# Kernel tuning notes

Hardware: AMD Instinct MI355X
Metric: run time of the kernel (lower is better)

The kernel has to match this reference:

```python
import jax, jax.numpy as jnp
import numpy as np

NUM_PM = 254
NUM_VM = 768
SEQ = NUM_PM + NUM_VM + 2  # 1024
H = 8
D = 256
DH = D // H
FF = 1024
L = 3
B = 8
PM_COV = 16
VM_COV = 16


def _ln(x, g, b, eps=1e-5):
    m = jnp.mean(x, axis=-1, keepdims=True)
    v = jnp.mean((x - m) ** 2, axis=-1, keepdims=True)
    return (x - m) * jax.lax.rsqrt(v + eps) * g + b


def setup_inputs() -> dict:
    key = jax.random.key(0)
    ks = jax.random.split(key, 32)
    n = lambda k, s: (jax.random.normal(k, s, dtype=jnp.float32) * 0.02)
    return {
        "vm_states": jax.random.normal(ks[0], (B, NUM_VM, VM_COV), dtype=jnp.float32),
        "num_step_states": jax.random.uniform(ks[1], (B, 1, 1), dtype=jnp.float32),
        "pm_states": jax.random.normal(ks[2], (B, NUM_PM, PM_COV), dtype=jnp.float32),
        "vm_pm_relation": jax.random.randint(ks[3], (B, SEQ - 2, 1), 0, NUM_PM),
        "num_vms_mask": jnp.zeros((B, NUM_VM), dtype=bool),
        "pm_W": n(ks[4], (PM_COV, D)), "pm_b": jnp.zeros((D,), jnp.float32),
        "vm_W": n(ks[5], (VM_COV, D)), "vm_b": jnp.zeros((D,), jnp.float32),
        "Wqkv": n(ks[6], (L, D, 3 * D)), "bqkv": jnp.zeros((L, 3 * D), jnp.float32),
        "Wo": n(ks[7], (L, D, D)), "bo": jnp.zeros((L, D), jnp.float32),
        "ln1_g": jnp.ones((L, D), jnp.float32), "ln1_b": jnp.zeros((L, D), jnp.float32),
        "ln2_g": jnp.ones((L, D), jnp.float32), "ln2_b": jnp.zeros((L, D), jnp.float32),
        "W1": n(ks[8], (L, D, FF)), "b1": jnp.zeros((L, FF), jnp.float32),
        "W2": n(ks[9], (L, FF, D)), "b2": jnp.zeros((L, D), jnp.float32),
        "out_W": n(ks[10], (D, 1)), "out_b": jnp.zeros((1,), jnp.float32),
        "crit_W": n(ks[11], (D, 1)), "crit_b": jnp.zeros((1,), jnp.float32),
    }


def reference(vm_states, num_step_states, pm_states, vm_pm_relation, num_vms_mask,
              pm_W, pm_b, vm_W, vm_b, Wqkv, bqkv, Wo, bo,
              ln1_g, ln1_b, ln2_g, ln2_b, W1, b1, W2, b2,
              out_W, out_b, crit_W, crit_b):
    b = vm_states.shape[0]
    # --- relation-based sparse mask: True = blocked ---
    r = vm_pm_relation[:, :, 0]                              # [b, SEQ-2]
    inner = r[:, :, None] != r[:, None, :]                   # [b, SEQ-2, SEQ-2]
    local = jnp.ones((b, SEQ, SEQ), dtype=bool)
    local = local.at[:, 0, 0].set(False)
    local = local.at[:, -1, -1].set(False)
    local = local.at[:, 1:-1, 1:-1].set(inner)
    pad = jnp.zeros((b, SEQ), dtype=bool).at[:, 1 + NUM_PM:-1].set(num_vms_mask)
    bias = jnp.where(local | pad[:, None, :], -1e9, 0.0)[:, None]  # [b,1,SEQ,SEQ]
    # --- encode ---
    src = jnp.concatenate([jnp.tile(num_step_states, (1, 1, D)),
                           pm_states @ pm_W + pm_b], axis=1)       # [b, NUM_PM+1, D]
    critic_tok = -jnp.ones((b, 1, D), dtype=vm_states.dtype)
    tgt = jnp.concatenate([vm_states @ vm_W + vm_b, critic_tok], axis=1)  # [b, NUM_VM+1, D]
    x = jnp.concatenate([src, tgt], axis=1)                   # [b, SEQ, D]
    scale = 1.0 / np.sqrt(DH)
    for i in range(L):
        # pre-norm masked self-attention
        h = _ln(x, ln1_g[i], ln1_b[i])
        qkv = h @ Wqkv[i] + bqkv[i]
        q, k, v = [t.reshape(b, SEQ, H, DH) for t in jnp.split(qkv, 3, axis=-1)]
        scores = jnp.einsum('bqhd,bkhd->bhqk', q, k) * scale + bias
        attn = jax.nn.softmax(scores, axis=-1)
        o = jnp.einsum('bhqk,bkhd->bqhd', attn, v).reshape(b, SEQ, D)
        x = x + o @ Wo[i] + bo[i]
        # pre-norm gelu FFN
        h2 = _ln(x, ln2_g[i], ln2_b[i])
        x = x + jax.nn.gelu(h2 @ W1[i] + b1[i]) @ W2[i] + b2[i]
    tgt_out = x[:, NUM_PM + 1:]                               # [b, NUM_VM+1, D]
    score = (tgt_out[:, :-1] @ out_W + out_b)[..., 0]         # [b, NUM_VM]
    critic_score = tgt_out[:, -1] @ crit_W + crit_b           # [b, 1]
    return jnp.concatenate([score, critic_score], axis=1)     # [b, NUM_VM+1]
```

## Files before the change

kernel.cpp:

```cpp
#include <hip/hip_runtime.h>
#include <hip/hip_bf16.h>
#include <math.h>

#define NUM_PM 254
#define NUM_VM 768
#define SEQQ   1024
#define NH     8
#define DD     256
#define DH     32
#define FF     1024
#define NB     8
#define MROWS  (NB*SEQQ)

typedef unsigned short u16;
typedef __attribute__((ext_vector_type(8))) short bf16x8;
typedef __attribute__((ext_vector_type(4))) float f32x4;

__device__ __forceinline__ float bf2f(u16 u){
    union { float f; unsigned int i; } c; c.i = ((unsigned int)u) << 16; return c.f;
}
__device__ __forceinline__ u16 f2bf(float f){
    union { float f; unsigned int u; } c; c.f = f;
    unsigned int r = c.u + 0x7FFFu + ((c.u >> 16) & 1u);
    return (u16)(r >> 16);
}
__device__ __forceinline__ float gelu_tanh(float x){
    float x3 = x*x*x;
    float t = tanhf(0.7978845608028654f*(x + 0.044715f*x3));
    return 0.5f*x*(1.0f+t);
}

#define GLOAD16(gp, lp) __builtin_amdgcn_global_load_lds( \
    (const __attribute__((address_space(1))) void*)(gp), \
    (__attribute__((address_space(3))) void*)(lp), 16, 0, 0)

__global__ void embed_kernel(const float* __restrict__ vm_states,
                             const float* __restrict__ num_step,
                             const float* __restrict__ pm_states,
                             const float* __restrict__ pm_W, const float* __restrict__ pm_b,
                             const float* __restrict__ vm_W, const float* __restrict__ vm_b,
                             float* __restrict__ x)
{
    int row = blockIdx.x*4 + (threadIdx.x>>6);
    int lane = threadIdx.x & 63;
    int b = row >> 10, s = row & 1023;
    int col = lane*4;
    float4 out;
    if (s == 0){
        float v = num_step[b]; out = (float4){v,v,v,v};
    } else if (s == SEQQ-1){
        out = (float4){-1.f,-1.f,-1.f,-1.f};
    } else {
        const float* in; const float* W; const float* bias;
        if (s <= NUM_PM){ in = pm_states + (size_t)(b*NUM_PM + s-1)*16; W = pm_W; bias = pm_b; }
        else            { in = vm_states + (size_t)(b*NUM_VM + (s-1-NUM_PM))*16; W = vm_W; bias = vm_b; }
        float4 i0 = *(const float4*)in,      i1 = *(const float4*)(in+4);
        float4 i2 = *(const float4*)(in+8),  i3 = *(const float4*)(in+12);
        float in16[16] = {i0.x,i0.y,i0.z,i0.w, i1.x,i1.y,i1.z,i1.w,
                          i2.x,i2.y,i2.z,i2.w, i3.x,i3.y,i3.z,i3.w};
        out = *(const float4*)&bias[col];
        #pragma unroll
        for (int k=0;k<16;k++){
            float4 w4 = *(const float4*)&W[k*DD + col];
            out.x = fmaf(in16[k], w4.x, out.x);
            out.y = fmaf(in16[k], w4.y, out.y);
            out.z = fmaf(in16[k], w4.z, out.z);
            out.w = fmaf(in16[k], w4.w, out.w);
        }
    }
    *(float4*)&x[(size_t)row*DD + col] = out;
}

__global__ void tcast_all_kernel(const float* __restrict__ Wqkv, const float* __restrict__ Wo,
                                 const float* __restrict__ W1,   const float* __restrict__ W2,
                                 u16* __restrict__ wq, u16* __restrict__ wo,
                                 u16* __restrict__ w1, u16* __restrict__ w2)
{
    __shared__ float t[32][33];
    int id = blockIdx.x;
    const float* in; u16* out; int K, N, layer, tile;
    if (id < 576)       { in=Wqkv; out=wq; K=256;  N=768;  layer=id/192; tile=id%192; }
    else if (id < 768)  { id-=576;  in=Wo; out=wo; K=256;  N=256;  layer=id/64;  tile=id%64;  }
    else if (id < 1536) { id-=768;  in=W1; out=w1; K=256;  N=1024; layer=id/256; tile=id%256; }
    else                { id-=1536; in=W2; out=w2; K=1024; N=256;  layer=id/256; tile=id%256; }
    int ntx = N/32;
    int n0 = (tile % ntx)*32, k0 = (tile / ntx)*32;
    size_t lofs = (size_t)layer * K * N;
    int tx = threadIdx.x & 31, ty = threadIdx.x >> 5;
    #pragma unroll
    for (int i=0;i<4;i++)
        t[ty + i*8][tx] = in[lofs + (size_t)(k0 + ty + i*8)*N + n0 + tx];
    __syncthreads();
    #pragma unroll
    for (int i=0;i<4;i++)
        out[lofs + (size_t)(n0 + ty + i*8)*K + k0 + tx] = f2bf(t[tx][ty + i*8]);
}

__global__ void ln_kernel(const float* __restrict__ x, const float* __restrict__ g,
                          const float* __restrict__ bta, u16* __restrict__ out)
{
    int row = blockIdx.x*4 + (threadIdx.x>>6);
    int lane = threadIdx.x & 63;
    const float4 v = *(const float4*)&x[(size_t)row*DD + lane*4];
    float s1 = v.x+v.y+v.z+v.w;
    float s2 = fmaf(v.x,v.x, fmaf(v.y,v.y, fmaf(v.z,v.z, v.w*v.w)));
    #pragma unroll
    for (int off=1; off<64; off<<=1){ s1 += __shfl_xor(s1,off); s2 += __shfl_xor(s2,off); }
    float m    = s1*(1.0f/DD);
    float var  = s2*(1.0f/DD) - m*m;
    float rstd = rsqrtf(var + 1e-5f);
    float4 g4 = *(const float4*)&g[lane*4];
    float4 b4 = *(const float4*)&bta[lane*4];
    short4 o;
    o.x = (short)f2bf((v.x-m)*rstd*g4.x + b4.x);
    o.y = (short)f2bf((v.y-m)*rstd*g4.y + b4.y);
    o.z = (short)f2bf((v.z-m)*rstd*g4.z + b4.z);
    o.w = (short)f2bf((v.w-m)*rstd*g4.w + b4.w);
    *(short4*)&out[(size_t)row*DD + lane*4] = o;
}

template<int EPI>
__launch_bounds__(256)
__global__ void mgemm_kernel(const u16* __restrict__ A, const u16* __restrict__ Bt,
                             const float* __restrict__ bias, u16* __restrict__ C,
                             int N, int K)
{
    __shared__ u16 As[2][128][32];
    __shared__ u16 Bs[2][128][32];
    int tid = threadIdx.x;
    int wid = tid >> 6, lane = tid & 63;
    int wr = wid >> 1, wc = wid & 1;
    int row0 = blockIdx.y*128, col0 = blockIdx.x*128;
    int l15 = lane & 15, lh = lane >> 4;

    int srow = wid*32 + (lane>>2);
    int skof = (lane&3)*8;
    const u16* Ag = A  + (size_t)(row0 + srow)*K + skof;
    const u16* Bg = Bt + (size_t)(col0 + srow)*K + skof;

#define STAGE_M(buf, k0) do{ \
    GLOAD16(Ag + (k0),          &As[buf][wid*32][0]);    \
    GLOAD16(Ag + (k0) + 16*K,   &As[buf][wid*32+16][0]); \
    GLOAD16(Bg + (k0),          &Bs[buf][wid*32][0]);    \
    GLOAD16(Bg + (k0) + 16*K,   &Bs[buf][wid*32+16][0]); }while(0)

    f32x4 acc[4][4] = {};
    int nk = K >> 5;
    STAGE_M(0, 0);
    __syncthreads();
    for (int kt = 0; kt < nk; kt++){
        int cur = kt & 1;
        if (kt+1 < nk) STAGE_M(cur^1, (kt+1)*32);
        bf16x8 af[4], bfv[4];
        #pragma unroll
        for (int f=0; f<4; f++){
            af[f]  = *(const bf16x8*)&As[cur][wr*64 + f*16 + l15][lh*8];
            bfv[f] = *(const bf16x8*)&Bs[cur][wc*64 + f*16 + l15][lh*8];
        }
        #pragma unroll
        for (int i=0;i<4;i++)
            #pragma unroll
            for (int j=0;j<4;j++)
                acc[i][j] = __builtin_amdgcn_mfma_f32_16x16x32_bf16(af[i], bfv[j], acc[i][j], 0,0,0);
        __syncthreads();
    }
#undef STAGE_M

    #pragma unroll
    for (int i=0;i<4;i++){
        #pragma unroll
        for (int j=0;j<4;j++){
            int col = col0 + wc*64 + j*16 + l15;
            float bb = bias[col];
            #pragma unroll
            for (int r=0;r<4;r++){
                int row = row0 + wr*64 + i*16 + lh*4 + r;
                float v = acc[i][j][r] + bb;
                if (EPI==2) v = gelu_tanh(v);
                C[(size_t)row*N + col] = f2bf(v);
            }
        }
    }
}

__launch_bounds__(256)
__global__ void mgemm2_kernel(const u16* __restrict__ A, const u16* __restrict__ Bt,
                              const float* __restrict__ bias, const float* __restrict__ res,
                              float* __restrict__ C, int N, int K)
{
    __shared__ u16 As[2][64][32];
    __shared__ u16 Bs[2][128][32];
    int tid = threadIdx.x;
    int wid = tid >> 6, lane = tid & 63;
    int wr = wid >> 1, wc = wid & 1;
    int row0 = blockIdx.y*64, col0 = blockIdx.x*128;
    int l15 = lane & 15, lh = lane >> 4;

    int srowA = wid*16 + (lane>>2);
    int srowB = wid*32 + (lane>>2);
    int skof  = (lane&3)*8;
    const u16* Ag = A  + (size_t)(row0 + srowA)*K + skof;
    const u16* Bg = Bt + (size_t)(col0 + srowB)*K + skof;

#define STAGE_M2(buf, k0) do{ \
    GLOAD16(Ag + (k0),          &As[buf][wid*16][0]);    \
    GLOAD16(Bg + (k0),          &Bs[buf][wid*32][0]);    \
    GLOAD16(Bg + (k0) + 16*K,   &Bs[buf][wid*32+16][0]); }while(0)

    f32x4 acc[2][4] = {};
    int nk = K >> 5;
    STAGE_M2(0, 0);
    __syncthreads();
    for (int kt = 0; kt < nk; kt++){
        int cur = kt & 1;
        if (kt+1 < nk) STAGE_M2(cur^1, (kt+1)*32);
        bf16x8 af[2], bfv[4];
        #pragma unroll
        for (int i=0;i<2;i++)
            af[i] = *(const bf16x8*)&As[cur][wr*32 + i*16 + l15][lh*8];
        #pragma unroll
        for (int j=0;j<4;j++)
            bfv[j] = *(const bf16x8*)&Bs[cur][wc*64 + j*16 + l15][lh*8];
        #pragma unroll
        for (int i=0;i<2;i++)
            #pragma unroll
            for (int j=0;j<4;j++)
                acc[i][j] = __builtin_amdgcn_mfma_f32_16x16x32_bf16(af[i], bfv[j], acc[i][j], 0,0,0);
        __syncthreads();
    }
#undef STAGE_M2

    #pragma unroll
    for (int i=0;i<2;i++){
        #pragma unroll
        for (int j=0;j<4;j++){
            int col = col0 + wc*64 + j*16 + l15;
            float bb = bias[col];
            #pragma unroll
            for (int r=0;r<4;r++){
                int row = row0 + wr*32 + i*16 + lh*4 + r;
                size_t idx = (size_t)row*N + col;
                C[idx] = acc[i][j][r] + bb + res[idx];
            }
        }
    }
}

__global__ void group_build_kernel(const int* __restrict__ rel, const unsigned char* __restrict__ mask,
                                   int* __restrict__ counts, int* __restrict__ offs,
                                   int* __restrict__ members)
{
    __shared__ int cntS[256], offS[256], wsum[4];
    int b = blockIdx.x, tid = threadIdx.x;
    if (tid < 256) cntS[tid] = 0;
    __syncthreads();
    int s = tid, c = -1, p = -1;
    bool valid = (s != 0) && (s != SEQQ-1);
    if (valid && s >= 1+NUM_PM && mask[b*NUM_VM + (s-1-NUM_PM)]) valid = false;
    if (valid){
        c = rel[b*(SEQQ-2) + s-1];
        p = atomicAdd(&cntS[c], 1);
    }
    __syncthreads();
    if (tid < 256){
        int v = cntS[tid];
        int incl = v;
        #pragma unroll
        for (int d=1; d<64; d<<=1){
            int n = __shfl_up(incl, d);
            if ((tid & 63) >= d) incl += n;
        }
        offS[tid] = incl - v;
        if ((tid & 63) == 63) wsum[tid>>6] = incl;
    }
    __syncthreads();
    if (tid < 256){
        int w = tid >> 6, base = 0;
        #pragma unroll
        for (int i=0;i<4;i++) if (i < w) base += wsum[i];
        offS[tid] += base;
    }
    __syncthreads();
    if (valid) members[b*SEQQ + offS[c] + p] = s;
    if (tid < 256){
        counts[b*256 + tid] = cntS[tid];
        offs[b*256 + tid]   = offS[tid];
    }
}

__launch_bounds__(256)
__global__ void attn_kernel(const u16* __restrict__ qkv, const int* __restrict__ rel,
                            const int* __restrict__ counts, const int* __restrict__ offs,
                            const int* __restrict__ members, u16* __restrict__ o)
{
    int gq = blockIdx.x*4 + (threadIdx.x >> 6);
    int lane = threadIdx.x & 63;
    int b = gq >> 10, s = gq & 1023;
    const float scale = 0.17677669529663687f;

    const u16* base = qkv + (size_t)(b*SEQQ + s)*768 + lane*4;
    short4 q4i = *(const short4*)base;
    float qx = bf2f((u16)q4i.x)*scale, qy = bf2f((u16)q4i.y)*scale,
          qz = bf2f((u16)q4i.z)*scale, qw = bf2f((u16)q4i.w)*scale;

    int cnt; const int* mlist = nullptr;
    if (s == 0 || s == SEQQ-1) { cnt = 1; }
    else {
        int c = rel[b*(SEQQ-2) + s-1];
        cnt   = counts[b*256 + c];
        mlist = members + b*SEQQ + offs[b*256 + c];
    }

    float m_run = -1e30f, l_run = 0.f;
    float ax=0.f, ay=0.f, az=0.f, aw=0.f;
    for (int j0 = 0; j0 < cnt; j0 += 4){
        short4 k4[4], v4[4];
        #pragma unroll
        for (int k=0;k<4;k++){
            int jj = j0 + k; jj = (jj < cnt) ? jj : (cnt-1);
            int mi = mlist ? mlist[jj] : s;
            const u16* kb = qkv + (size_t)(b*SEQQ + mi)*768 + 256 + lane*4;
            k4[k] = *(const short4*)kb;
            v4[k] = *(const short4*)(kb + 256);
        }
        #pragma unroll
        for (int k=0;k<4;k++){
            if (j0 + k < cnt){
                float sc = qx*bf2f((u16)k4[k].x) + qy*bf2f((u16)k4[k].y)
                         + qz*bf2f((u16)k4[k].z) + qw*bf2f((u16)k4[k].w);
                sc += __shfl_xor(sc, 1);
                sc += __shfl_xor(sc, 2);
                sc += __shfl_xor(sc, 4);
                float mn = fmaxf(m_run, sc);
                float corr = __expf(m_run - mn);
                float p = __expf(sc - mn);
                l_run = l_run*corr + p;
                ax = ax*corr + p*bf2f((u16)v4[k].x);
                ay = ay*corr + p*bf2f((u16)v4[k].y);
                az = az*corr + p*bf2f((u16)v4[k].z);
                aw = aw*corr + p*bf2f((u16)v4[k].w);
                m_run = mn;
            }
        }
    }
    float inv = (l_run > 0.f) ? 1.0f/l_run : 0.f;
    u16* orow = o + (size_t)(b*SEQQ + s)*DD + lane*4;
    short4 outv;
    outv.x = (short)f2bf(ax*inv); outv.y = (short)f2bf(ay*inv);
    outv.z = (short)f2bf(az*inv); outv.w = (short)f2bf(aw*inv);
    *(short4*)orow = outv;
}

__global__ void out_kernel(const float* __restrict__ x,
                           const float* __restrict__ out_W, const float* __restrict__ out_b,
                           const float* __restrict__ crit_W, const float* __restrict__ crit_b,
                           float* __restrict__ out)
{
    int gidx = blockIdx.x*4 + (threadIdx.x>>6);
    int lane = threadIdx.x & 63;
    if (gidx >= NB*769) return;
    int b = gidx / 769, j = gidx % 769;
    int srow; const float* Wp; float bb;
    if (j < 768){ srow = b*SEQQ + 1 + NUM_PM + j; Wp = out_W; bb = out_b[0]; }
    else        { srow = b*SEQQ + SEQQ-1;         Wp = crit_W; bb = crit_b[0]; }
    const float* xr = x + (size_t)srow*DD;
    float4 xv = *(const float4*)&xr[lane*4];
    float4 wv = *(const float4*)&Wp[lane*4];
    float sdot = xv.x*wv.x + xv.y*wv.y + xv.z*wv.z + xv.w*wv.w;
    #pragma unroll
    for (int off=32; off; off>>=1) sdot += __shfl_down(sdot, off);
    if (lane==0) out[gidx] = sdot + bb;
}

extern "C" void kernel_launch(void* const* d_in, const int* in_sizes, int n_in,
                              void* d_out, int out_size, void* d_ws, size_t ws_size,
                              hipStream_t stream)
{
    const float* vm_states = (const float*)d_in[0];
    const float* num_step  = (const float*)d_in[1];
    const float* pm_states = (const float*)d_in[2];
    const int*   rel       = (const int*)d_in[3];
    const unsigned char* mask = (const unsigned char*)d_in[4];
    const float* pm_W = (const float*)d_in[5];
    const float* pm_b = (const float*)d_in[6];
    const float* vm_W = (const float*)d_in[7];
    const float* vm_b = (const float*)d_in[8];
    const float* Wqkv = (const float*)d_in[9];
    const float* bqkv = (const float*)d_in[10];
    const float* Wo   = (const float*)d_in[11];
    const float* bo   = (const float*)d_in[12];
    const float* ln1g = (const float*)d_in[13];
    const float* ln1b = (const float*)d_in[14];
    const float* ln2g = (const float*)d_in[15];
    const float* ln2b = (const float*)d_in[16];
    const float* W1   = (const float*)d_in[17];
    const float* b1   = (const float*)d_in[18];
    const float* W2   = (const float*)d_in[19];
    const float* b2   = (const float*)d_in[20];
    const float* out_W = (const float*)d_in[21];
    const float* out_b = (const float*)d_in[22];
    const float* crit_W = (const float*)d_in[23];
    const float* crit_b = (const float*)d_in[24];

    char* ws = (char*)d_ws;
    const size_t MB = 1024*1024;
    float* x    = (float*)(ws);
    u16*   hbuf = (u16*)(ws + 8*MB);
    u16*   aout = (u16*)(ws + 12*MB);
    u16*   qkv  = (u16*)(ws + 16*MB);
    u16*   ff1  = (u16*)(ws + 28*MB);
    u16*   wq   = (u16*)(ws + 44*MB);
    u16*   wo   = wq + (size_t)3*768*256;
    u16*   w1   = wo + (size_t)3*256*256;
    u16*   w2   = w1 + (size_t)3*1024*256;
    int*   counts  = (int*)(ws + 50*MB);
    int*   offs    = counts + NB*256;
    int*   members = offs   + NB*256;

    tcast_all_kernel<<<2304, 256, 0, stream>>>(Wqkv, Wo, W1, W2, wq, wo, w1, w2);
    group_build_kernel<<<NB, 1024, 0, stream>>>(rel, mask, counts, offs, members);
    embed_kernel<<<MROWS/4, 256, 0, stream>>>(vm_states, num_step, pm_states,
                                              pm_W, pm_b, vm_W, vm_b, x);
    for (int i=0;i<3;i++){
        ln_kernel<<<MROWS/4,256,0,stream>>>(x, ln1g + i*DD, ln1b + i*DD, hbuf);
        mgemm_kernel<0><<<dim3(768/128, MROWS/128),256,0,stream>>>(
            hbuf, wq + (size_t)i*768*256, bqkv + i*768, qkv, 768, 256);
        attn_kernel<<<MROWS/4, 256, 0, stream>>>(qkv, rel, counts, offs, members, aout);
        mgemm2_kernel<<<dim3(256/128, MROWS/64),256,0,stream>>>(
            aout, wo + (size_t)i*256*256, bo + i*DD, x, x, 256, 256);
        ln_kernel<<<MROWS/4,256,0,stream>>>(x, ln2g + i*DD, ln2b + i*DD, hbuf);
        mgemm_kernel<2><<<dim3(1024/128, MROWS/128),256,0,stream>>>(
            hbuf, w1 + (size_t)i*1024*256, b1 + i*FF, ff1, 1024, 256);
        mgemm2_kernel<<<dim3(256/128, MROWS/64),256,0,stream>>>(
            ff1, w2 + (size_t)i*256*1024, b2 + i*DD, x, x, 256, 1024);
    }
    out_kernel<<<(NB*769+3)/4, 256, 0, stream>>>(x, out_W, out_b, crit_W, crit_b, (float*)d_out);
}
```

Before: 350.2 us.

## Fuse LayerNorm into embedding and residual GEMM epilogues with full-row tiles

```diff
diff --git a/kernel.cpp b/kernel.cpp
--- a/kernel.cpp
+++ b/kernel.cpp
@@ -34,12 +34,13 @@
     (const __attribute__((address_space(1))) void*)(gp), \
     (__attribute__((address_space(3))) void*)(lp), 16, 0, 0)
 
-__global__ void embed_kernel(const float* __restrict__ vm_states,
-                             const float* __restrict__ num_step,
-                             const float* __restrict__ pm_states,
-                             const float* __restrict__ pm_W, const float* __restrict__ pm_b,
-                             const float* __restrict__ vm_W, const float* __restrict__ vm_b,
-                             float* __restrict__ x)
+__global__ void embed_ln_kernel(const float* __restrict__ vm_states,
+                                const float* __restrict__ num_step,
+                                const float* __restrict__ pm_states,
+                                const float* __restrict__ pm_W, const float* __restrict__ pm_b,
+                                const float* __restrict__ vm_W, const float* __restrict__ vm_b,
+                                const float* __restrict__ g, const float* __restrict__ beta,
+                                float* __restrict__ x, u16* __restrict__ h)
 {
     int row = blockIdx.x*4 + (threadIdx.x>>6);
     int lane = threadIdx.x & 63;
@@ -69,6 +70,21 @@
         }
     }
     *(float4*)&x[(size_t)row*DD + col] = out;
+    float s1 = out.x+out.y+out.z+out.w;
+    float s2 = fmaf(out.x,out.x, fmaf(out.y,out.y, fmaf(out.z,out.z, out.w*out.w)));
+    #pragma unroll
+    for (int off=1; off<64; off<<=1){ s1 += __shfl_xor(s1,off); s2 += __shfl_xor(s2,off); }
+    float m    = s1*(1.0f/DD);
+    float var  = s2*(1.0f/DD) - m*m;
+    float rstd = rsqrtf(var + 1e-5f);
+    float4 g4 = *(const float4*)&g[col];
+    float4 b4 = *(const float4*)&beta[col];
+    short4 o;
+    o.x = (short)f2bf((out.x-m)*rstd*g4.x + b4.x);
+    o.y = (short)f2bf((out.y-m)*rstd*g4.y + b4.y);
+    o.z = (short)f2bf((out.z-m)*rstd*g4.z + b4.z);
+    o.w = (short)f2bf((out.w-m)*rstd*g4.w + b4.w);
+    *(short4*)&h[(size_t)row*DD + col] = o;
 }
 
 __global__ void tcast_all_kernel(const float* __restrict__ Wqkv, const float* __restrict__ Wo,
@@ -96,29 +112,6 @@
         out[lofs + (size_t)(n0 + ty + i*8)*K + k0 + tx] = f2bf(t[tx][ty + i*8]);
 }
 
-__global__ void ln_kernel(const float* __restrict__ x, const float* __restrict__ g,
-                          const float* __restrict__ bta, u16* __restrict__ out)
-{
-    int row = blockIdx.x*4 + (threadIdx.x>>6);
-    int lane = threadIdx.x & 63;
-    const float4 v = *(const float4*)&x[(size_t)row*DD + lane*4];
-    float s1 = v.x+v.y+v.z+v.w;
-    float s2 = fmaf(v.x,v.x, fmaf(v.y,v.y, fmaf(v.z,v.z, v.w*v.w)));
-    #pragma unroll
-    for (int off=1; off<64; off<<=1){ s1 += __shfl_xor(s1,off); s2 += __shfl_xor(s2,off); }
-    float m    = s1*(1.0f/DD);
-    float var  = s2*(1.0f/DD) - m*m;
-    float rstd = rsqrtf(var + 1e-5f);
-    float4 g4 = *(const float4*)&g[lane*4];
-    float4 b4 = *(const float4*)&bta[lane*4];
-    short4 o;
-    o.x = (short)f2bf((v.x-m)*rstd*g4.x + b4.x);
-    o.y = (short)f2bf((v.y-m)*rstd*g4.y + b4.y);
-    o.z = (short)f2bf((v.z-m)*rstd*g4.z + b4.z);
-    o.w = (short)f2bf((v.w-m)*rstd*g4.w + b4.w);
-    *(short4*)&out[(size_t)row*DD + lane*4] = o;
-}
-
 template<int EPI>
 __launch_bounds__(256)
 __global__ void mgemm_kernel(const u16* __restrict__ A, const u16* __restrict__ Bt,
@@ -183,44 +176,45 @@
     }
 }
 
+template<int LN_OUT>
 __launch_bounds__(256)
-__global__ void mgemm2_kernel(const u16* __restrict__ A, const u16* __restrict__ Bt,
-                              const float* __restrict__ bias, const float* __restrict__ res,
-                              float* __restrict__ C, int N, int K)
-{
-    __shared__ u16 As[2][64][32];
-    __shared__ u16 Bs[2][128][32];
+__global__ void mgemm2ln_kernel(const u16* __restrict__ A, const u16* __restrict__ Bt,
+                                const float* __restrict__ bias,
+                                const float* __restrict__ g, const float* __restrict__ beta,
+                                float* __restrict__ x, u16* __restrict__ h, int K)
+{
+    __shared__ u16 As[2][32][32];
+    __shared__ u16 Bs[2][256][32];
+    __shared__ float part1[32][4], part2[32][4];
     int tid = threadIdx.x;
     int wid = tid >> 6, lane = tid & 63;
-    int wr = wid >> 1, wc = wid & 1;
-    int row0 = blockIdx.y*64, col0 = blockIdx.x*128;
+    int row0 = blockIdx.x*32;
     int l15 = lane & 15, lh = lane >> 4;
 
-    int srowA = wid*16 + (lane>>2);
-    int srowB = wid*32 + (lane>>2);
-    int skof  = (lane&3)*8;
-    const u16* Ag = A  + (size_t)(row0 + srowA)*K + skof;
-    const u16* Bg = Bt + (size_t)(col0 + srowB)*K + skof;
-
-#define STAGE_M2(buf, k0) do{ \
-    GLOAD16(Ag + (k0),          &As[buf][wid*16][0]);    \
-    GLOAD16(Bg + (k0),          &Bs[buf][wid*32][0]);    \
-    GLOAD16(Bg + (k0) + 16*K,   &Bs[buf][wid*32+16][0]); }while(0)
+    const u16* Ag = A + (size_t)(row0 + wid*16 + (lane>>2))*K + (lane&3)*8;
+    const u16* Bg = Bt + (size_t)(wid*64 + (lane>>2))*K + (lane&3)*8;
+
+#define STAGE_L(buf, k0) do{ \
+    if (wid < 2) GLOAD16(Ag + (k0), &As[buf][wid*16][0]); \
+    GLOAD16(Bg + (k0),          &Bs[buf][wid*64][0]);     \
+    GLOAD16(Bg + (k0) + 16*K,   &Bs[buf][wid*64+16][0]);  \
+    GLOAD16(Bg + (k0) + 32*K,   &Bs[buf][wid*64+32][0]);  \
+    GLOAD16(Bg + (k0) + 48*K,   &Bs[buf][wid*64+48][0]);  }while(0)
 
     f32x4 acc[2][4] = {};
     int nk = K >> 5;
-    STAGE_M2(0, 0);
+    STAGE_L(0, 0);
     __syncthreads();
     for (int kt = 0; kt < nk; kt++){
         int cur = kt & 1;
-        if (kt+1 < nk) STAGE_M2(cur^1, (kt+1)*32);
+        if (kt+1 < nk) STAGE_L(cur^1, (kt+1)*32);
         bf16x8 af[2], bfv[4];
         #pragma unroll
         for (int i=0;i<2;i++)
-            af[i] = *(const bf16x8*)&As[cur][wr*32 + i*16 + l15][lh*8];
+            af[i] = *(const bf16x8*)&As[cur][i*16 + l15][lh*8];
         #pragma unroll
         for (int j=0;j<4;j++)
-            bfv[j] = *(const bf16x8*)&Bs[cur][wc*64 + j*16 + l15][lh*8];
+            bfv[j] = *(const bf16x8*)&Bs[cur][wid*64 + j*16 + l15][lh*8];
         #pragma unroll
         for (int i=0;i<2;i++)
             #pragma unroll
@@ -228,19 +222,61 @@
                 acc[i][j] = __builtin_amdgcn_mfma_f32_16x16x32_bf16(af[i], bfv[j], acc[i][j], 0,0,0);
         __syncthreads();
     }
-#undef STAGE_M2
-
+#undef STAGE_L
+
+    float s1a[2][4] = {}, s2a[2][4] = {};
     #pragma unroll
     for (int i=0;i<2;i++){
         #pragma unroll
         for (int j=0;j<4;j++){
-            int col = col0 + wc*64 + j*16 + l15;
+            int col = wid*64 + j*16 + l15;
             float bb = bias[col];
             #pragma unroll
             for (int r=0;r<4;r++){
-                int row = row0 + wr*32 + i*16 + lh*4 + r;
-                size_t idx = (size_t)row*N + col;
-                C[idx] = acc[i][j][r] + bb + res[idx];
+                int row = row0 + i*16 + lh*4 + r;
+                size_t idx = (size_t)row*DD + col;
+                float v = acc[i][j][r] + bb + x[idx];
+                x[idx] = v;
+                acc[i][j][r] = v;
+                if (LN_OUT){
+                    s1a[i][r] += v;
+                    s2a[i][r] = fmaf(v, v, s2a[i][r]);
+                }
+            }
+        }
+    }
+    if (LN_OUT){
+        #pragma unroll
+        for (int i=0;i<2;i++)
+            #pragma unroll
+            for (int r=0;r<4;r++){
+                float s1 = s1a[i][r], s2 = s2a[i][r];
+                s1 += __shfl_xor(s1,1); s2 += __shfl_xor(s2,1);
+                s1 += __shfl_xor(s1,2); s2 += __shfl_xor(s2,2);
+                s1 += __shfl_xor(s1,4); s2 += __shfl_xor(s2,4);
+                s1 += __shfl_xor(s1,8); s2 += __shfl_xor(s2,8);
+                if (l15 == 0){
+                    part1[i*16 + lh*4 + r][wid] = s1;
+                    part2[i*16 + lh*4 + r][wid] = s2;
+                }
+            }
+        __syncthreads();
+        #pragma unroll
+        for (int i=0;i<2;i++){
+            #pragma unroll
+            for (int r=0;r<4;r++){
+                int rl = i*16 + lh*4 + r;
+                float s1 = part1[rl][0]+part1[rl][1]+part1[rl][2]+part1[rl][3];
+                float s2 = part2[rl][0]+part2[rl][1]+part2[rl][2]+part2[rl][3];
+                float m    = s1*(1.0f/DD);
+                float var  = s2*(1.0f/DD) - m*m;
+                float rstd = rsqrtf(var + 1e-5f);
+                #pragma unroll
+                for (int j=0;j<4;j++){
+                    int col = wid*64 + j*16 + l15;
+                    float hv = (acc[i][j][r]-m)*rstd*g[col] + beta[col];
+                    h[(size_t)(row0+rl)*DD + col] = f2bf(hv);
+                }
             }
         }
     }
@@ -419,20 +455,23 @@
 
     tcast_all_kernel<<<2304, 256, 0, stream>>>(Wqkv, Wo, W1, W2, wq, wo, w1, w2);
     group_build_kernel<<<NB, 1024, 0, stream>>>(rel, mask, counts, offs, members);
-    embed_kernel<<<MROWS/4, 256, 0, stream>>>(vm_states, num_step, pm_states,
-                                              pm_W, pm_b, vm_W, vm_b, x);
+    embed_ln_kernel<<<MROWS/4, 256, 0, stream>>>(vm_states, num_step, pm_states,
+                                                 pm_W, pm_b, vm_W, vm_b,
+                                                 ln1g, ln1b, x, hbuf);
     for (int i=0;i<3;i++){
-        ln_kernel<<<MROWS/4,256,0,stream>>>(x, ln1g + i*DD, ln1b + i*DD, hbuf);
         mgemm_kernel<0><<<dim3(768/128, MROWS/128),256,0,stream>>>(
             hbuf, wq + (size_t)i*768*256, bqkv + i*768, qkv, 768, 256);
         attn_kernel<<<MROWS/4, 256, 0, stream>>>(qkv, rel, counts, offs, members, aout);
-        mgemm2_kernel<<<dim3(256/128, MROWS/64),256,0,stream>>>(
-            aout, wo + (size_t)i*256*256, bo + i*DD, x, x, 256, 256);
-        ln_kernel<<<MROWS/4,256,0,stream>>>(x, ln2g + i*DD, ln2b + i*DD, hbuf);
+        mgemm2ln_kernel<1><<<MROWS/32,256,0,stream>>>(
+            aout, wo + (size_t)i*256*256, bo + i*DD, ln2g + i*DD, ln2b + i*DD, x, hbuf, 256);
         mgemm_kernel<2><<<dim3(1024/128, MROWS/128),256,0,stream>>>(
             hbuf, w1 + (size_t)i*1024*256, b1 + i*FF, ff1, 1024, 256);
-        mgemm2_kernel<<<dim3(256/128, MROWS/64),256,0,stream>>>(
-            ff1, w2 + (size_t)i*256*1024, b2 + i*DD, x, x, 256, 1024);
+        if (i < 2)
+            mgemm2ln_kernel<1><<<MROWS/32,256,0,stream>>>(
+                ff1, w2 + (size_t)i*256*1024, b2 + i*DD, ln1g + (i+1)*DD, ln1b + (i+1)*DD, x, hbuf, 1024);
+        else
+            mgemm2ln_kernel<0><<<MROWS/32,256,0,stream>>>(
+                ff1, w2 + (size_t)i*256*1024, b2 + i*DD, nullptr, nullptr, x, nullptr, 1024);
     }
     out_kernel<<<(NB*769+3)/4, 256, 0, stream>>>(x, out_W, out_b, crit_W, crit_b, (float*)d_out);
 }
```

After: 361.6 us. +3.2%, slower.

## Merge prologue kernels, fuse output head into final GEMM, retile residual GEMMs

Applied to the files above, without the earlier changes.

```diff
diff --git a/kernel.cpp b/kernel.cpp
--- a/kernel.cpp
+++ b/kernel.cpp
@@ -34,66 +34,128 @@
     (const __attribute__((address_space(1))) void*)(gp), \
     (__attribute__((address_space(3))) void*)(lp), 16, 0, 0)
 
-__global__ void embed_kernel(const float* __restrict__ vm_states,
-                             const float* __restrict__ num_step,
-                             const float* __restrict__ pm_states,
-                             const float* __restrict__ pm_W, const float* __restrict__ pm_b,
-                             const float* __restrict__ vm_W, const float* __restrict__ vm_b,
-                             float* __restrict__ x)
-{
-    int row = blockIdx.x*4 + (threadIdx.x>>6);
-    int lane = threadIdx.x & 63;
-    int b = row >> 10, s = row & 1023;
-    int col = lane*4;
-    float4 out;
-    if (s == 0){
-        float v = num_step[b]; out = (float4){v,v,v,v};
-    } else if (s == SEQQ-1){
-        out = (float4){-1.f,-1.f,-1.f,-1.f};
+__global__ void prologue_kernel(const float* __restrict__ Wqkv, const float* __restrict__ Wo,
+                                const float* __restrict__ W1,   const float* __restrict__ W2,
+                                u16* __restrict__ wq, u16* __restrict__ wo,
+                                u16* __restrict__ w1, u16* __restrict__ w2,
+                                const int* __restrict__ rel, const unsigned char* __restrict__ mask,
+                                int* __restrict__ counts, int* __restrict__ offs,
+                                int* __restrict__ members,
+                                const float* __restrict__ vm_states,
+                                const float* __restrict__ num_step,
+                                const float* __restrict__ pm_states,
+                                const float* __restrict__ pm_W, const float* __restrict__ pm_b,
+                                const float* __restrict__ vm_W, const float* __restrict__ vm_b,
+                                const float* __restrict__ g, const float* __restrict__ beta,
+                                float* __restrict__ x, u16* __restrict__ h)
+{
+    __shared__ float t[32][33];
+    __shared__ int cntS[256], offS[256], wsum4[4];
+    int bid = blockIdx.x;
+    int tid = threadIdx.x;
+    if (bid < 2304){
+        int id = bid;
+        const float* in; u16* out; int K, N, layer, tile;
+        if (id < 576)       { in=Wqkv; out=wq; K=256;  N=768;  layer=id/192; tile=id%192; }
+        else if (id < 768)  { id-=576;  in=Wo; out=wo; K=256;  N=256;  layer=id/64;  tile=id%64;  }
+        else if (id < 1536) { id-=768;  in=W1; out=w1; K=256;  N=1024; layer=id/256; tile=id%256; }
+        else                { id-=1536; in=W2; out=w2; K=1024; N=256;  layer=id/256; tile=id%256; }
+        int ntx = N/32;
+        int n0 = (tile % ntx)*32, k0 = (tile / ntx)*32;
+        size_t lofs = (size_t)layer * K * N;
+        int tx = tid & 31, ty = tid >> 5;
+        #pragma unroll
+        for (int i=0;i<4;i++)
+            t[ty + i*8][tx] = in[lofs + (size_t)(k0 + ty + i*8)*N + n0 + tx];
+        __syncthreads();
+        #pragma unroll
+        for (int i=0;i<4;i++)
+            out[lofs + (size_t)(n0 + ty + i*8)*K + k0 + tx] = f2bf(t[tx][ty + i*8]);
+    } else if (bid < 2312){
+        int b = bid - 2304;
+        cntS[tid] = 0;
+        __syncthreads();
+        int myc[4], myp[4];
+        #pragma unroll
+        for (int si=0; si<4; si++){
+            int s = si*256 + tid;
+            bool valid = (s != 0) && (s != SEQQ-1);
+            if (valid && s >= 1+NUM_PM && mask[b*NUM_VM + (s-1-NUM_PM)]) valid = false;
+            myc[si] = -1;
+            if (valid){
+                myc[si] = rel[b*(SEQQ-2) + s-1];
+                myp[si] = atomicAdd(&cntS[myc[si]], 1);
+            }
+        }
+        __syncthreads();
+        int v = cntS[tid];
+        int incl = v;
+        #pragma unroll
+        for (int d=1; d<64; d<<=1){
+            int n = __shfl_up(incl, d);
+            if ((tid & 63) >= d) incl += n;
+        }
+        offS[tid] = incl - v;
+        if ((tid & 63) == 63) wsum4[tid>>6] = incl;
+        __syncthreads();
+        {
+            int w = tid >> 6, base = 0;
+            #pragma unroll
+            for (int i=0;i<4;i++) if (i < w) base += wsum4[i];
+            offS[tid] += base;
+        }
+        __syncthreads();
+        #pragma unroll
+        for (int si=0; si<4; si++)
+            if (myc[si] >= 0)
+                members[b*SEQQ + offS[myc[si]] + myp[si]] = si*256 + tid;
+        counts[b*256 + tid] = cntS[tid];
+        offs[b*256 + tid]   = offS[tid];
     } else {
-        const float* in; const float* W; const float* bias;
-        if (s <= NUM_PM){ in = pm_states + (size_t)(b*NUM_PM + s-1)*16; W = pm_W; bias = pm_b; }
-        else            { in = vm_states + (size_t)(b*NUM_VM + (s-1-NUM_PM))*16; W = vm_W; bias = vm_b; }
-        float4 i0 = *(const float4*)in,      i1 = *(const float4*)(in+4);
-        float4 i2 = *(const float4*)(in+8),  i3 = *(const float4*)(in+12);
-        float in16[16] = {i0.x,i0.y,i0.z,i0.w, i1.x,i1.y,i1.z,i1.w,
-                          i2.x,i2.y,i2.z,i2.w, i3.x,i3.y,i3.z,i3.w};
-        out = *(const float4*)&bias[col];
-        #pragma unroll
-        for (int k=0;k<16;k++){
-            float4 w4 = *(const float4*)&W[k*DD + col];
-            out.x = fmaf(in16[k], w4.x, out.x);
-            out.y = fmaf(in16[k], w4.y, out.y);
-            out.z = fmaf(in16[k], w4.z, out.z);
-            out.w = fmaf(in16[k], w4.w, out.w);
-        }
-    }
-    *(float4*)&x[(size_t)row*DD + col] = out;
-}
-
-__global__ void tcast_all_kernel(const float* __restrict__ Wqkv, const float* __restrict__ Wo,
-                                 const float* __restrict__ W1,   const float* __restrict__ W2,
-                                 u16* __restrict__ wq, u16* __restrict__ wo,
-                                 u16* __restrict__ w1, u16* __restrict__ w2)
-{
-    __shared__ float t[32][33];
-    int id = blockIdx.x;
-    const float* in; u16* out; int K, N, layer, tile;
-    if (id < 576)       { in=Wqkv; out=wq; K=256;  N=768;  layer=id/192; tile=id%192; }
-    else if (id < 768)  { id-=576;  in=Wo; out=wo; K=256;  N=256;  layer=id/64;  tile=id%64;  }
-    else if (id < 1536) { id-=768;  in=W1; out=w1; K=256;  N=1024; layer=id/256; tile=id%256; }
-    else                { id-=1536; in=W2; out=w2; K=1024; N=256;  layer=id/256; tile=id%256; }
-    int ntx = N/32;
-    int n0 = (tile % ntx)*32, k0 = (tile / ntx)*32;
-    size_t lofs = (size_t)layer * K * N;
-    int tx = threadIdx.x & 31, ty = threadIdx.x >> 5;
-    #pragma unroll
-    for (int i=0;i<4;i++)
-        t[ty + i*8][tx] = in[lofs + (size_t)(k0 + ty + i*8)*N + n0 + tx];
-    __syncthreads();
-    #pragma unroll
-    for (int i=0;i<4;i++)
-        out[lofs + (size_t)(n0 + ty + i*8)*K + k0 + tx] = f2bf(t[tx][ty + i*8]);
+        int row = (bid - 2312)*4 + (tid>>6);
+        int lane = tid & 63;
+        int b = row >> 10, s = row & 1023;
+        int col = lane*4;
+        float4 out;
+        if (s == 0){
+            float v = num_step[b]; out = (float4){v,v,v,v};
+        } else if (s == SEQQ-1){
+            out = (float4){-1.f,-1.f,-1.f,-1.f};
+        } else {
+            const float* in; const float* W; const float* bias;
+            if (s <= NUM_PM){ in = pm_states + (size_t)(b*NUM_PM + s-1)*16; W = pm_W; bias = pm_b; }
+            else            { in = vm_states + (size_t)(b*NUM_VM + (s-1-NUM_PM))*16; W = vm_W; bias = vm_b; }
+            float4 i0 = *(const float4*)in,      i1 = *(const float4*)(in+4);
+            float4 i2 = *(const float4*)(in+8),  i3 = *(const float4*)(in+12);
+            float in16[16] = {i0.x,i0.y,i0.z,i0.w, i1.x,i1.y,i1.z,i1.w,
+                              i2.x,i2.y,i2.z,i2.w, i3.x,i3.y,i3.z,i3.w};
+            out = *(const float4*)&bias[col];
+            #pragma unroll
+            for (int k=0;k<16;k++){
+                float4 w4 = *(const float4*)&W[k*DD + col];
+                out.x = fmaf(in16[k], w4.x, out.x);
+                out.y = fmaf(in16[k], w4.y, out.y);
+                out.z = fmaf(in16[k], w4.z, out.z);
+                out.w = fmaf(in16[k], w4.w, out.w);
+            }
+        }
+        *(float4*)&x[(size_t)row*DD + col] = out;
+        float s1 = out.x+out.y+out.z+out.w;
+        float s2 = fmaf(out.x,out.x, fmaf(out.y,out.y, fmaf(out.z,out.z, out.w*out.w)));
+        #pragma unroll
+        for (int off=1; off<64; off<<=1){ s1 += __shfl_xor(s1,off); s2 += __shfl_xor(s2,off); }
+        float m    = s1*(1.0f/DD);
+        float var  = s2*(1.0f/DD) - m*m;
+        float rstd = rsqrtf(var + 1e-5f);
+        float4 g4 = *(const float4*)&g[col];
+        float4 b4 = *(const float4*)&beta[col];
+        short4 o;
+        o.x = (short)f2bf((out.x-m)*rstd*g4.x + b4.x);
+        o.y = (short)f2bf((out.y-m)*rstd*g4.y + b4.y);
+        o.z = (short)f2bf((out.z-m)*rstd*g4.z + b4.z);
+        o.w = (short)f2bf((out.w-m)*rstd*g4.w + b4.w);
+        *(short4*)&h[(size_t)row*DD + col] = o;
+    }
 }
 
 __global__ void ln_kernel(const float* __restrict__ x, const float* __restrict__ g,
@@ -119,7 +181,65 @@
     *(short4*)&out[(size_t)row*DD + lane*4] = o;
 }
 
-template<int EPI>
+__launch_bounds__(256)
+__global__ void qgemm_kernel(const u16* __restrict__ A, const u16* __restrict__ Bt,
+                             const float* __restrict__ bias, u16* __restrict__ C,
+                             int N, int K)
+{
+    __shared__ u16 As[2][64][32];
+    __shared__ u16 Bs[2][128][32];
+    int tid = threadIdx.x;
+    int wid = tid >> 6, lane = tid & 63;
+    int wr = wid >> 1, wc = wid & 1;
+    int row0 = blockIdx.y*64, col0 = blockIdx.x*128;
+    int l15 = lane & 15, lh = lane >> 4;
+
+    const u16* Ag = A  + (size_t)(row0 + wid*16 + (lane>>2))*K + (lane&3)*8;
+    const u16* Bg = Bt + (size_t)(col0 + wid*32 + (lane>>2))*K + (lane&3)*8;
+
+#define STAGE_Q(buf, k0) do{ \
+    GLOAD16(Ag + (k0),          &As[buf][wid*16][0]);    \
+    GLOAD16(Bg + (k0),          &Bs[buf][wid*32][0]);    \
+    GLOAD16(Bg + (k0) + 16*K,   &Bs[buf][wid*32+16][0]); }while(0)
+
+    f32x4 acc[2][4] = {};
+    int nk = K >> 5;
+    STAGE_Q(0, 0);
+    __syncthreads();
+    for (int kt = 0; kt < nk; kt++){
+        int cur = kt & 1;
+        if (kt+1 < nk) STAGE_Q(cur^1, (kt+1)*32);
+        bf16x8 af[2], bfv[4];
+        #pragma unroll
+        for (int i=0;i<2;i++)
+            af[i] = *(const bf16x8*)&As[cur][wr*32 + i*16 + l15][lh*8];
+        #pragma unroll
+        for (int j=0;j<4;j++)
+            bfv[j] = *(const bf16x8*)&Bs[cur][wc*64 + j*16 + l15][lh*8];
+        #pragma unroll
+        for (int i=0;i<2;i++)
+            #pragma unroll
+            for (int j=0;j<4;j++)
+                acc[i][j] = __builtin_amdgcn_mfma_f32_16x16x32_bf16(af[i], bfv[j], acc[i][j], 0,0,0);
+        __syncthreads();
+    }
+#undef STAGE_Q
+
+    #pragma unroll
+    for (int i=0;i<2;i++){
+        #pragma unroll
+        for (int j=0;j<4;j++){
+            int col = col0 + wc*64 + j*16 + l15;
+            float bb = bias[col];
+            #pragma unroll
+            for (int r=0;r<4;r++){
+                int row = row0 + wr*32 + i*16 + lh*4 + r;
+                C[(size_t)row*N + col] = f2bf(acc[i][j][r] + bb);
+            }
+        }
+    }
+}
+
 __launch_bounds__(256)
 __global__ void mgemm_kernel(const u16* __restrict__ A, const u16* __restrict__ Bt,
                              const float* __restrict__ bias, u16* __restrict__ C,
@@ -133,10 +253,8 @@
     int row0 = blockIdx.y*128, col0 = blockIdx.x*128;
     int l15 = lane & 15, lh = lane >> 4;
 
-    int srow = wid*32 + (lane>>2);
-    int skof = (lane&3)*8;
-    const u16* Ag = A  + (size_t)(row0 + srow)*K + skof;
-    const u16* Bg = Bt + (size_t)(col0 + srow)*K + skof;
+    const u16* Ag = A  + (size_t)(row0 + wid*32 + (lane>>2))*K + (lane&3)*8;
+    const u16* Bg = Bt + (size_t)(col0 + wid*32 + (lane>>2))*K + (lane&3)*8;
 
 #define STAGE_M(buf, k0) do{ \
     GLOAD16(Ag + (k0),          &As[buf][wid*32][0]);    \
@@ -175,116 +293,94 @@
             #pragma unroll
             for (int r=0;r<4;r++){
                 int row = row0 + wr*64 + i*16 + lh*4 + r;
-                float v = acc[i][j][r] + bb;
-                if (EPI==2) v = gelu_tanh(v);
-                C[(size_t)row*N + col] = f2bf(v);
-            }
-        }
-    }
-}
-
+                C[(size_t)row*N + col] = f2bf(gelu_tanh(acc[i][j][r] + bb));
+            }
+        }
+    }
+}
+
+template<int HEAD>
 __launch_bounds__(256)
-__global__ void mgemm2_kernel(const u16* __restrict__ A, const u16* __restrict__ Bt,
-                              const float* __restrict__ bias, const float* __restrict__ res,
-                              float* __restrict__ C, int N, int K)
+__global__ void mgemm64_kernel(const u16* __restrict__ A, const u16* __restrict__ Bt,
+                               const float* __restrict__ bias, float* __restrict__ x,
+                               const float* __restrict__ out_W, const float* __restrict__ out_b,
+                               const float* __restrict__ crit_W, const float* __restrict__ crit_b,
+                               float* __restrict__ out, int K)
 {
     __shared__ u16 As[2][64][32];
-    __shared__ u16 Bs[2][128][32];
+    __shared__ u16 Bs[2][64][32];
     int tid = threadIdx.x;
     int wid = tid >> 6, lane = tid & 63;
     int wr = wid >> 1, wc = wid & 1;
-    int row0 = blockIdx.y*64, col0 = blockIdx.x*128;
+    int row0 = blockIdx.y*64, col0 = blockIdx.x*64;
     int l15 = lane & 15, lh = lane >> 4;
 
-    int srowA = wid*16 + (lane>>2);
-    int srowB = wid*32 + (lane>>2);
-    int skof  = (lane&3)*8;
-    const u16* Ag = A  + (size_t)(row0 + srowA)*K + skof;
-    const u16* Bg = Bt + (size_t)(col0 + srowB)*K + skof;
-
-#define STAGE_M2(buf, k0) do{ \
-    GLOAD16(Ag + (k0),          &As[buf][wid*16][0]);    \
-    GLOAD16(Bg + (k0),          &Bs[buf][wid*32][0]);    \
-    GLOAD16(Bg + (k0) + 16*K,   &Bs[buf][wid*32+16][0]); }while(0)
-
-    f32x4 acc[2][4] = {};
+    const u16* Ag = A  + (size_t)(row0 + wid*16 + (lane>>2))*K + (lane&3)*8;
+    const u16* Bg = Bt + (size_t)(col0 + wid*16 + (lane>>2))*K + (lane&3)*8;
+
+#define STAGE_S(buf, k0) do{ \
+    GLOAD16(Ag + (k0), &As[buf][wid*16][0]); \
+    GLOAD16(Bg + (k0), &Bs[buf][wid*16][0]); }while(0)
+
+    f32x4 acc[2][2] = {};
     int nk = K >> 5;
-    STAGE_M2(0, 0);
+    STAGE_S(0, 0);
     __syncthreads();
     for (int kt = 0; kt < nk; kt++){
         int cur = kt & 1;
-        if (kt+1 < nk) STAGE_M2(cur^1, (kt+1)*32);
-        bf16x8 af[2], bfv[4];
+        if (kt+1 < nk) STAGE_S(cur^1, (kt+1)*32);
+        bf16x8 af[2], bfv[2];
         #pragma unroll
         for (int i=0;i<2;i++)
             af[i] = *(const bf16x8*)&As[cur][wr*32 + i*16 + l15][lh*8];
         #pragma unroll
-        for (int j=0;j<4;j++)
-            bfv[j] = *(const bf16x8*)&Bs[cur][wc*64 + j*16 + l15][lh*8];
+        for (int j=0;j<2;j++)
+            bfv[j] = *(const bf16x8*)&Bs[cur][wc*32 + j*16 + l15][lh*8];
         #pragma unroll
         for (int i=0;i<2;i++)
             #pragma unroll
-            for (int j=0;j<4;j++)
+            for (int j=0;j<2;j++)
                 acc[i][j] = __builtin_amdgcn_mfma_f32_16x16x32_bf16(af[i], bfv[j], acc[i][j], 0,0,0);
         __syncthreads();
     }
-#undef STAGE_M2
+#undef STAGE_S
 
     #pragma unroll
     for (int i=0;i<2;i++){
         #pragma unroll
-        for (int j=0;j<4;j++){
-            int col = col0 + wc*64 + j*16 + l15;
-            float bb = bias[col];
-            #pragma unroll
-            for (int r=0;r<4;r++){
-                int row = row0 + wr*32 + i*16 + lh*4 + r;
-                size_t idx = (size_t)row*N + col;
-                C[idx] = acc[i][j][r] + bb + res[idx];
-            }
-        }
-    }
-}
-
-__global__ void group_build_kernel(const int* __restrict__ rel, const unsigned char* __restrict__ mask,
-                                   int* __restrict__ counts, int* __restrict__ offs,
-                                   int* __restrict__ members)
-{
-    __shared__ int cntS[256], offS[256], wsum[4];
-    int b = blockIdx.x, tid = threadIdx.x;
-    if (tid < 256) cntS[tid] = 0;
-    __syncthreads();
-    int s = tid, c = -1, p = -1;
-    bool valid = (s != 0) && (s != SEQQ-1);
-    if (valid && s >= 1+NUM_PM && mask[b*NUM_VM + (s-1-NUM_PM)]) valid = false;
-    if (valid){
-        c = rel[b*(SEQQ-2) + s-1];
-        p = atomicAdd(&cntS[c], 1);
-    }
-    __syncthreads();
-    if (tid < 256){
-        int v = cntS[tid];
-        int incl = v;
-        #pragma unroll
-        for (int d=1; d<64; d<<=1){
-            int n = __shfl_up(incl, d);
-            if ((tid & 63) >= d) incl += n;
-        }
-        offS[tid] = incl - v;
-        if ((tid & 63) == 63) wsum[tid>>6] = incl;
-    }
-    __syncthreads();
-    if (tid < 256){
-        int w = tid >> 6, base = 0;
-        #pragma unroll
-        for (int i=0;i<4;i++) if (i < w) base += wsum[i];
-        offS[tid] += base;
-    }
-    __syncthreads();
-    if (valid) members[b*SEQQ + offS[c] + p] = s;
-    if (tid < 256){
-        counts[b*256 + tid] = cntS[tid];
-        offs[b*256 + tid]   = offS[tid];
+        for (int r=0;r<4;r++){
+            int row = row0 + wr*32 + i*16 + lh*4 + r;
+            float hp = 0.f;
+            bool do_head = false;
+            int s = row & 1023;
+            #pragma unroll
+            for (int j=0;j<2;j++){
+                int col = col0 + wc*32 + j*16 + l15;
+                size_t idx = (size_t)row*DD + col;
+                float v = acc[i][j][r] + bias[col] + x[idx];
+                x[idx] = v;
+                if (HEAD){
+                    float w = (s == 1023) ? crit_W[col] : out_W[col];
+                    hp = fmaf(v, w, hp);
+                }
+            }
+            if (HEAD && s >= 1 + NUM_PM){
+                do_head = true;
+                hp += __shfl_xor(hp, 1);
+                hp += __shfl_xor(hp, 2);
+                hp += __shfl_xor(hp, 4);
+                hp += __shfl_xor(hp, 8);
+                if (l15 == 0){
+                    int b = row >> 10;
+                    int jj = (s == 1023) ? 768 : (s - (1 + NUM_PM));
+                    float add = hp;
+                    if (blockIdx.x == 0 && wc == 0)
+                        add += (s == 1023) ? crit_b[0] : out_b[0];
+                    atomicAdd(&out[b*769 + jj], add);
+                }
+            }
+            (void)do_head;
+        }
     }
 }
 
@@ -349,27 +445,6 @@
     outv.x = (short)f2bf(ax*inv); outv.y = (short)f2bf(ay*inv);
     outv.z = (short)f2bf(az*inv); outv.w = (short)f2bf(aw*inv);
     *(short4*)orow = outv;
-}
-
-__global__ void out_kernel(const float* __restrict__ x,
-                           const float* __restrict__ out_W, const float* __restrict__ out_b,
-                           const float* __restrict__ crit_W, const float* __restrict__ crit_b,
-                           float* __restrict__ out)
-{
-    int gidx = blockIdx.x*4 + (threadIdx.x>>6);
-    int lane = threadIdx.x & 63;
-    if (gidx >= NB*769) return;
-    int b = gidx / 769, j = gidx % 769;
-    int srow; const float* Wp; float bb;
-    if (j < 768){ srow = b*SEQQ + 1 + NUM_PM + j; Wp = out_W; bb = out_b[0]; }
-    else        { srow = b*SEQQ + SEQQ-1;         Wp = crit_W; bb = crit_b[0]; }
-    const float* xr = x + (size_t)srow*DD;
-    float4 xv = *(const float4*)&xr[lane*4];
-    float4 wv = *(const float4*)&Wp[lane*4];
-    float sdot = xv.x*wv.x + xv.y*wv.y + xv.z*wv.z + xv.w*wv.w;
-    #pragma unroll
-    for (int off=32; off; off>>=1) sdot += __shfl_down(sdot, off);
-    if (lane==0) out[gidx] = sdot + bb;
 }
 
 extern "C" void kernel_launch(void* const* d_in, const int* in_sizes, int n_in,
@@ -417,22 +492,31 @@
     int*   offs    = counts + NB*256;
     int*   members = offs   + NB*256;
 
-    tcast_all_kernel<<<2304, 256, 0, stream>>>(Wqkv, Wo, W1, W2, wq, wo, w1, w2);
-    group_build_kernel<<<NB, 1024, 0, stream>>>(rel, mask, counts, offs, members);
-    embed_kernel<<<MROWS/4, 256, 0, stream>>>(vm_states, num_step, pm_states,
-                                              pm_W, pm_b, vm_W, vm_b, x);
+    hipMemsetAsync(d_out, 0, (size_t)out_size*sizeof(float), stream);
+    prologue_kernel<<<4360, 256, 0, stream>>>(Wqkv, Wo, W1, W2, wq, wo, w1, w2,
+                                              rel, mask, counts, offs, members,
+                                              vm_states, num_step, pm_states,
+                                              pm_W, pm_b, vm_W, vm_b,
+                                              ln1g, ln1b, x, hbuf);
     for (int i=0;i<3;i++){
-        ln_kernel<<<MROWS/4,256,0,stream>>>(x, ln1g + i*DD, ln1b + i*DD, hbuf);
-        mgemm_kernel<0><<<dim3(768/128, MROWS/128),256,0,stream>>>(
+        qgemm_kernel<<<dim3(768/128, MROWS/64),256,0,stream>>>(
             hbuf, wq + (size_t)i*768*256, bqkv + i*768, qkv, 768, 256);
         attn_kernel<<<MROWS/4, 256, 0, stream>>>(qkv, rel, counts, offs, members, aout);
-        mgemm2_kernel<<<dim3(256/128, MROWS/64),256,0,stream>>>(
-            aout, wo + (size_t)i*256*256, bo + i*DD, x, x, 256, 256);
+        mgemm64_kernel<0><<<dim3(256/64, MROWS/64),256,0,stream>>>(
+            aout, wo + (size_t)i*256*256, bo + i*DD, x,
+            nullptr, nullptr, nullptr, nullptr, nullptr, 256);
         ln_kernel<<<MROWS/4,256,0,stream>>>(x, ln2g + i*DD, ln2b + i*DD, hbuf);
-        mgemm_kernel<2><<<dim3(1024/128, MROWS/128),256,0,stream>>>(
+        mgemm_kernel<<<dim3(1024/128, MROWS/128),256,0,stream>>>(
             hbuf, w1 + (size_t)i*1024*256, b1 + i*FF, ff1, 1024, 256);
-        mgemm2_kernel<<<dim3(256/128, MROWS/64),256,0,stream>>>(
-            ff1, w2 + (size_t)i*256*1024, b2 + i*DD, x, x, 256, 1024);
-    }
-    out_kernel<<<(NB*769+3)/4, 256, 0, stream>>>(x, out_W, out_b, crit_W, crit_b, (float*)d_out);
-}
+        if (i < 2){
+            mgemm64_kernel<0><<<dim3(256/64, MROWS/64),256,0,stream>>>(
+                ff1, w2 + (size_t)i*256*1024, b2 + i*DD, x,
+                nullptr, nullptr, nullptr, nullptr, nullptr, 1024);
+            ln_kernel<<<MROWS/4,256,0,stream>>>(x, ln1g + (i+1)*DD, ln1b + (i+1)*DD, hbuf);
+        } else {
+            mgemm64_kernel<1><<<dim3(256/64, MROWS/64),256,0,stream>>>(
+                ff1, w2 + (size_t)i*256*1024, b2 + i*DD, x,
+                out_W, out_b, crit_W, crit_b, (float*)d_out, 1024);
+        }
+    }
+}
```

After: 332.9 us. -5.0%, faster.
